# Optimization experiments

Hardware: AMD Instinct MI355X
Metric: run time of the kernel (lower is better)

The kernel has to match this reference:

```python
import jax, jax.numpy as jnp
import numpy as np

N = 50000          # num nodes
E = 800000         # num edges
MUL = 32           # channel multiplicity per irrep
NB = 8             # number of radial basis functions
R_MAX = 1.0
AVG = 16.0         # avg_num_neighbors
SQ3 = 3.0 ** 0.5


def setup_inputs() -> dict:
    key = jax.random.key(0)
    k = jax.random.split(key, 12)
    inp = {
        "node_feats": jax.random.normal(k[0], (N, 4 * MUL), dtype=jnp.float32),   # 32x0e + 32x1o (mul_ir layout)
        "edge_vec": jax.random.normal(k[1], (E, 3), dtype=jnp.float32),
        "edge_length": jax.random.uniform(k[2], (E,), dtype=jnp.float32),
        "senders": jax.random.randint(k[3], (E,), 0, N, dtype=jnp.int32),
        "receivers": jax.random.randint(k[4], (E,), 0, N, dtype=jnp.int32),
        "num_nodes": N,
        # linear_up: per-irrep channel mixing (scalars, vectors)
        "W_up0": jax.random.normal(k[5], (MUL, MUL), dtype=jnp.float32),
        "W_up1": jax.random.normal(k[6], (MUL, MUL), dtype=jnp.float32),
        # radial MLP: NB -> 64 -> 64 -> weight_numel (4 paths * MUL)
        "mlp_w0": jax.random.normal(k[7], (NB, 64), dtype=jnp.float32) / NB ** 0.5,
        "mlp_b0": jnp.zeros((64,), dtype=jnp.float32),
        "mlp_w1": jax.random.normal(k[8], (64, 64), dtype=jnp.float32) / 8.0,
        "mlp_b1": jnp.zeros((64,), dtype=jnp.float32),
        "mlp_w2": jax.random.normal(k[9], (64, 4 * MUL), dtype=jnp.float32) / 8.0,
        "mlp_b2": jnp.zeros((4 * MUL,), dtype=jnp.float32),
        # final linear: mid irreps 64x0e + 64x1o -> 32x0e + 32x1o
        "W_out0": jax.random.normal(k[10], (2 * MUL, MUL), dtype=jnp.float32),
        "W_out1": jax.random.normal(k[11], (2 * MUL, MUL), dtype=jnp.float32),
    }
    return inp


def _radial_embedding(r):
    # gaussian soft-one-hot, matches _radial_embedding(function_type='gaussian')
    x = jnp.clip(r / R_MAX, 0.0, 1.0)
    centers = jnp.arange(NB, dtype=jnp.float32) / (NB - 1)
    sigma = 1.0 / (NB - 1)
    emb = jnp.exp(-0.5 * ((x[:, None] - centers[None, :]) / sigma) ** 2)
    emb = emb * (NB ** 0.5) * (r <= R_MAX).astype(jnp.float32)[:, None]
    return emb  # [E, NB]


def reference(node_feats, edge_vec, edge_length, senders, receivers, num_nodes,
              W_up0, W_up1, mlp_w0, mlp_b0, mlp_w1, mlp_b1, mlp_w2, mlp_b2,
              W_out0, W_out1):
    f32 = jnp.float32
    # --- edge spherical harmonics (lmax=1, normalize=True, component norm) ---
    rhat = edge_vec / (jnp.linalg.norm(edge_vec, axis=-1, keepdims=True) + 1e-12)
    Y1 = SQ3 * rhat                                             # [E,3]
    # --- radial weights ---
    emb = _radial_embedding(edge_length)                        # [E,NB]
    h = jax.nn.silu(emb @ mlp_w0 + mlp_b0)
    h = jax.nn.silu(h @ mlp_w1 + mlp_b1)
    w = (h @ mlp_w2 + mlp_b2).reshape(-1, 4, MUL)               # [E,4,MUL] per-path per-channel
    # --- linear_up (per-irrep channel mixing, fan-in normalized) ---
    s = node_feats[:, :MUL]                                     # [N,MUL] scalars 0e
    v = node_feats[:, MUL:].reshape(-1, MUL, 3)                 # [N,MUL,3] vectors 1o
    xs = (s @ W_up0) / f32(MUL) ** 0.5                          # [N,MUL]
    xv = jnp.einsum('nmc,mk->nkc', v, W_up1) / f32(MUL) ** 0.5  # [N,MUL,3]
    # --- gather senders ---
    ss = xs[senders]                                            # [E,MUL]
    vv = xv[senders]                                            # [E,MUL,3]
    # --- channelwise tensor product paths (filter = {0e,1o}) ---
    m0 = w[:, 0] * ss                                           # 0e x 0e -> 0e   [E,MUL]
    m1 = w[:, 1][:, :, None] * ss[:, :, None] * Y1[:, None, :]  # 0e x 1o -> 1o   [E,MUL,3]
    m2 = w[:, 2][:, :, None] * vv                               # 1o x 0e -> 1o   [E,MUL,3]
    m3 = w[:, 3] * (jnp.einsum('emc,ec->em', vv, Y1) / SQ3)     # 1o x 1o -> 0e   [E,MUL]
    mid_s = jnp.concatenate([m0, m3], axis=1)                   # [E,2*MUL]
    mid_v = jnp.concatenate([m1, m2], axis=1)                   # [E,2*MUL,3]
    # --- scatter-sum to receivers ---
    msg_s = jax.ops.segment_sum(mid_s, receivers, num_segments=num_nodes)   # [N,2*MUL]
    msg_v = jax.ops.segment_sum(mid_v, receivers, num_segments=num_nodes)   # [N,2*MUL,3]
    # --- final per-irrep linear ---
    out_s = (msg_s @ W_out0) / f32(2 * MUL) ** 0.5              # [N,MUL]
    out_v = jnp.einsum('nmc,mk->nkc', msg_v, W_out1) / f32(2 * MUL) ** 0.5  # [N,MUL,3]
    out = jnp.concatenate([out_s, out_v.reshape(-1, 3 * MUL)], axis=1)      # [N,4*MUL]
    return out / max(AVG, 1e-8)
```

## Files before the change

### kernel.cpp

```cpp
#include <hip/hip_runtime.h>
#include <math.h>

#define SQ3F   1.7320508075688772f
#define SQRT8F 2.8284271247461903f
#define OSCALE (1.0f / 128.0f)

__device__ __forceinline__ float fast_silu(float x) {
    return x * __builtin_amdgcn_rcpf(1.0f + __expf(-x));
}

__global__ __launch_bounds__(256) void tr_kernel(const float* __restrict__ w2,
                                                 float* __restrict__ w2t) {
    const int t = blockIdx.x * 256 + threadIdx.x;
    if (t < 8192) {
        const int o = t >> 6, i = t & 63;
        w2t[t] = w2[i * 128 + o];
    }
}

__global__ __launch_bounds__(256) void up_kernel(const float* __restrict__ nf,
                                                 const float* __restrict__ Wu0,
                                                 const float* __restrict__ Wu1,
                                                 float* __restrict__ xall, int N) {
    __shared__ float sW0[1024], sW1[1024];
    for (int i = threadIdx.x; i < 1024; i += 256) { sW0[i] = Wu0[i]; sW1[i] = Wu1[i]; }
    __syncthreads();
    const int t = blockIdx.x * 256 + threadIdx.x;
    const int n = t >> 5, k = t & 31;
    if (n >= N) return;
    const float* row = nf + (size_t)n * 128;
    float a0 = 0.f, a1 = 0.f, a2 = 0.f, a3 = 0.f;
#pragma unroll
    for (int m = 0; m < 32; ++m) {
        const float wa = sW0[m * 32 + k], wb = sW1[m * 32 + k];
        a0 += row[m] * wa;
        a1 += row[32 + m * 3 + 0] * wb;
        a2 += row[32 + m * 3 + 1] * wb;
        a3 += row[32 + m * 3 + 2] * wb;
    }
    const float s = 0.17677669529663687f;
    float4 o; o.x = a0 * s; o.y = a1 * s; o.z = a2 * s; o.w = a3 * s;
    reinterpret_cast<float4*>(xall)[(size_t)n * 32 + k] = o;
}

__global__ __launch_bounds__(256) void hist_kernel(const int* __restrict__ rcv,
                                                   int* __restrict__ cnt, int E) {
    const int t = blockIdx.x * 256 + threadIdx.x;
    if (t < E) atomicAdd(&cnt[rcv[t]], 1);
}

__global__ __launch_bounds__(1024) void scan_kernel(const int* __restrict__ cnt,
                                                    int* __restrict__ off, int N, int E) {
    __shared__ int part[1024];
    const int t = threadIdx.x;
    const int CH = (N + 1023) / 1024;
    const int lo = t * CH;
    const int hi = (lo + CH < N) ? lo + CH : N;
    int s = 0;
    for (int i = lo; i < hi; ++i) s += cnt[i];
    part[t] = s;
    __syncthreads();
    for (int d = 1; d < 1024; d <<= 1) {
        const int v = (t >= d) ? part[t - d] : 0;
        __syncthreads();
        part[t] += v;
        __syncthreads();
    }
    int run = (t > 0) ? part[t - 1] : 0;
    for (int i = lo; i < hi; ++i) { off[i] = run; run += cnt[i]; }
    if (t == 0) off[N] = E;
}

__global__ __launch_bounds__(256) void scat_kernel(const int* __restrict__ rcv,
                                                   const int* __restrict__ off,
                                                   int* __restrict__ cur,
                                                   int* __restrict__ sid, int E) {
    const int t = blockIdx.x * 256 + threadIdx.x;
    if (t < E) {
        const int r = rcv[t];
        const int p = off[r] + atomicAdd(&cur[r], 1);
        sid[p] = t;
    }
}

__global__ __launch_bounds__(256) void wassign_kernel(const int* __restrict__ off,
                                                      int* __restrict__ wlo,
                                                      int* __restrict__ whi,
                                                      int N, int NW) {
    const int n = blockIdx.x * 256 + threadIdx.x;
    if (n < N) {
        int w = off[n] >> 6;
        if (w >= NW) w = NW - 1;
        atomicMin(&wlo[w], n);
        atomicMax(&whi[w], n);
    }
}

__global__ __launch_bounds__(64, 2) void ek4(const float* __restrict__ edge_vec,
                                             const float* __restrict__ edge_len,
                                             const int*  __restrict__ senders,
                                             const int*  __restrict__ receivers,
                                             const int*  __restrict__ sid,
                                             const int*  __restrict__ off,
                                             const int*  __restrict__ wlo,
                                             const int*  __restrict__ whi,
                                             const float* __restrict__ w0,
                                             const float* __restrict__ b0,
                                             const float* __restrict__ w1,
                                             const float* __restrict__ b1,
                                             const float* __restrict__ b2,
                                             const float* __restrict__ w2t,
                                             const float* __restrict__ Wo0,
                                             const float* __restrict__ Wo1,
                                             const float4* __restrict__ xall,
                                             float* __restrict__ outp,
                                             int E) {
    __shared__ float st[64][65];
    __shared__ int   rcvt[64];
    const int lane = threadIdx.x;
    const int w = blockIdx.x;
    const int nlo = wlo[w], nhi = whi[w];
    if (nhi < nlo) return;
    const int estart = off[nlo], eend = off[nhi + 1];
    if (estart >= eend) return;

    int   rprev = -1;
    float accA = 0.f, accB = 0.f;

    for (int bs = estart; bs < eend; bs += 64) {
        const int nv = (eend - bs < 64) ? (eend - bs) : 64;
        const int sp = (lane < nv) ? (bs + lane) : (eend - 1);
        const int e  = sid[sp];
        rcvt[lane] = receivers[e];

        const float ev0 = edge_vec[e * 3 + 0];
        const float ev1 = edge_vec[e * 3 + 1];
        const float ev2 = edge_vec[e * 3 + 2];
        const float r   = edge_len[e];
        const int  snd  = senders[e];

        const float nrm = sqrtf(ev0 * ev0 + ev1 * ev1 + ev2 * ev2) + 1e-12f;
        const float sc  = SQ3F * __builtin_amdgcn_rcpf(nrm);
        const float Y0 = ev0 * sc, Y1 = ev1 * sc, Y2 = ev2 * sc;

        const float xcl  = fminf(fmaxf(r, 0.0f), 1.0f);
        const float gate = (r <= 1.0f) ? SQRT8F : 0.0f;
        float emb[8];
#pragma unroll
        for (int i = 0; i < 8; ++i) {
            const float d = xcl * 7.0f - (float)i;
            emb[i] = __expf(-0.5f * d * d) * gate;
        }

        float h0[64];
#pragma unroll
        for (int o = 0; o < 64; ++o) {
            float a = b0[o];
#pragma unroll
            for (int i = 0; i < 8; ++i) a += emb[i] * w0[i * 64 + o];
            h0[o] = fast_silu(a);
        }

#pragma unroll 1
        for (int ob = 0; ob < 64; ob += 8) {
            float a[8];
#pragma unroll
            for (int u = 0; u < 8; ++u) a[u] = b1[ob + u];
#pragma unroll
            for (int i = 0; i < 64; ++i) {
                const float hv = h0[i];
#pragma unroll
                for (int u = 0; u < 8; ++u) a[u] += hv * w1[i * 64 + ob + u];
            }
#pragma unroll
            for (int u = 0; u < 8; ++u) st[ob + u][lane] = fast_silu(a[u]);
        }

        const float4* xrow = xall + (size_t)snd * 32;
        float outS[32], tA[32], oV[96];
#pragma unroll
        for (int k = 0; k < 32; ++k) { outS[k] = 0.f; tA[k] = 0.f; }
#pragma unroll
        for (int k = 0; k < 96; ++k) oV[k] = 0.f;

#pragma unroll 1
        for (int m = 0; m < 32; ++m) {
            const float* r0 = w2t + m * 64;
            const float* r1 = w2t + (32 + m) * 64;
            const float* r2 = w2t + (64 + m) * 64;
            const float* r3 = w2t + (96 + m) * 64;
            float d0 = b2[m], d1 = b2[32 + m], d2 = b2[64 + m], d3 = b2[96 + m];
#pragma unroll
            for (int i = 0; i < 64; ++i) {
                const float hv = st[i][lane];
                d0 += hv * r0[i]; d1 += hv * r1[i];
                d2 += hv * r2[i]; d3 += hv * r3[i];
            }
            const float4 g = xrow[m];
            const float ss = g.x;
            const float dv = g.y * Y0 + g.z * Y1 + g.w * Y2;
            const float a0 = d0 * ss;
            const float a3 = d3 * dv * (1.0f / SQ3F);
            const float t1 = d1 * ss;
            const float p0 = d2 * g.y, p1 = d2 * g.z, p2 = d2 * g.w;
            const float* wa = Wo0 + m * 32;
            const float* wb = Wo0 + (32 + m) * 32;
            const float* wc = Wo1 + m * 32;
            const float* wd = Wo1 + (32 + m) * 32;
#pragma unroll
            for (int k = 0; k < 32; ++k) {
                outS[k] += a0 * wa[k] + a3 * wb[k];
                tA[k]   += t1 * wc[k];
                const float wv = wd[k];
                oV[k * 3 + 0] += p0 * wv;
                oV[k * 3 + 1] += p1 * wv;
                oV[k * 3 + 2] += p2 * wv;
            }
        }
#pragma unroll
        for (int k = 0; k < 32; ++k) {
            oV[k * 3 + 0] += tA[k] * Y0;
            oV[k * 3 + 1] += tA[k] * Y1;
            oV[k * 3 + 2] += tA[k] * Y2;
        }

#pragma unroll
        for (int j = 0; j < 32; ++j) st[j][lane]      = outS[j];
#pragma unroll
        for (int j = 0; j < 32; ++j) st[32 + j][lane] = oV[j];
        __syncthreads();
        if (rprev < 0) rprev = rcvt[0];
        {
            int rA = rprev; float a = accA;
            for (int ee = 0; ee < nv; ++ee) {
                const int rc = rcvt[ee];
                if (rc != rA) {
                    outp[(size_t)rA * 128 + lane] = a * OSCALE;
                    a = 0.f; rA = rc;
                }
                a += st[lane][ee];
            }
            accA = a;
        }
        __syncthreads();

#pragma unroll
        for (int j = 0; j < 64; ++j) st[j][lane] = oV[32 + j];
        __syncthreads();
        {
            int rB = rprev; float b = accB;
            for (int ee = 0; ee < nv; ++ee) {
                const int rc = rcvt[ee];
                if (rc != rB) {
                    outp[(size_t)rB * 128 + 64 + lane] = b * OSCALE;
                    b = 0.f; rB = rc;
                }
                b += st[lane][ee];
            }
            accB = b; rprev = rB;
        }
        __syncthreads();
    }

    outp[(size_t)rprev * 128 + lane]      = accA * OSCALE;
    outp[(size_t)rprev * 128 + 64 + lane] = accB * OSCALE;
}

extern "C" void kernel_launch(void* const* d_in, const int* in_sizes, int n_in,
                              void* d_out, int out_size, void* d_ws, size_t ws_size,
                              hipStream_t stream) {
    const float* node_feats = (const float*)d_in[0];
    const float* edge_vec   = (const float*)d_in[1];
    const float* edge_len   = (const float*)d_in[2];
    const int*   senders    = (const int*)d_in[3];
    const int*   receivers  = (const int*)d_in[4];
    const float* W_up0  = (const float*)d_in[6];
    const float* W_up1  = (const float*)d_in[7];
    const float* mlp_w0 = (const float*)d_in[8];
    const float* mlp_b0 = (const float*)d_in[9];
    const float* mlp_w1 = (const float*)d_in[10];
    const float* mlp_b1 = (const float*)d_in[11];
    const float* mlp_w2 = (const float*)d_in[12];
    const float* mlp_b2 = (const float*)d_in[13];
    const float* W_out0 = (const float*)d_in[14];
    const float* W_out1 = (const float*)d_in[15];

    const int N  = in_sizes[0] / 128;
    const int E  = in_sizes[1] / 3;
    const int NW = (E + 63) / 64;

    float* xall = (float*)d_ws;
    float* w2t  = xall + (size_t)N * 128;
    int*   cnt  = (int*)(w2t + 8192);
    int*   off  = cnt + N;
    int*   cur  = off + N + 1;
    int*   sid  = cur + N;
    int*   wlo  = sid + E;
    int*   whi  = wlo + NW;

    tr_kernel<<<32, 256, 0, stream>>>(mlp_w2, w2t);
    up_kernel<<<(N * 32 + 255) / 256, 256, 0, stream>>>(node_feats, W_up0, W_up1, xall, N);

    hipMemsetAsync(cnt, 0, (size_t)(3 * N + 1) * sizeof(int), stream);
    hist_kernel<<<(E + 255) / 256, 256, 0, stream>>>(receivers, cnt, E);
    scan_kernel<<<1, 1024, 0, stream>>>(cnt, off, N, E);
    scat_kernel<<<(E + 255) / 256, 256, 0, stream>>>(receivers, off, cur, sid, E);

    hipMemsetAsync(wlo, 0x7f, (size_t)NW * sizeof(int), stream);
    hipMemsetAsync(whi, 0xff, (size_t)NW * sizeof(int), stream);
    wassign_kernel<<<(N + 255) / 256, 256, 0, stream>>>(off, wlo, whi, N, NW);

    hipMemsetAsync(d_out, 0, (size_t)out_size * sizeof(float), stream);
    ek4<<<NW, 64, 0, stream>>>(edge_vec, edge_len, senders, receivers, sid, off,
                               wlo, whi,
                               mlp_w0, mlp_b0, mlp_w1, mlp_b1, mlp_b2,
                               w2t, W_out0, W_out1,
                               (const float4*)xall, (float*)d_out, E);
}
```

Measured before the change: 2.495 ms.

## Keep hidden layer in registers and split output accumulation into two passes

The second MLP hidden layer h1 now stays in registers instead of going through shared memory, so the third MLP layer reads registers rather than LDS. The per-channel loop is split into two passes. The first pass builds the scalar outputs and the tA term, and the second pass recomputes the d2 path and builds the vector outputs. This avoids keeping outS, tA and all 96 oV accumulators live at the same time. It adds 64 live registers for h1, re-reads xrow, and adds an extra barrier, so register pressure at the launch bound of (64, 2) could cause spills.

New measurement: 3.274 ms. +31.2%, slower.

```diff
diff --git a/kernel.cpp b/kernel.cpp
--- a/kernel.cpp
+++ b/kernel.cpp
@@ -96,7 +96,7 @@
     }
 }
 
-__global__ __launch_bounds__(64, 2) void ek4(const float* __restrict__ edge_vec,
+__global__ __launch_bounds__(64, 2) void ek5(const float* __restrict__ edge_vec,
                                              const float* __restrict__ edge_len,
                                              const int*  __restrict__ senders,
                                              const int*  __restrict__ receivers,
@@ -161,7 +161,8 @@
             h0[o] = fast_silu(a);
         }
 
-#pragma unroll 1
+        float h1[64];
+#pragma unroll
         for (int ob = 0; ob < 64; ob += 8) {
             float a[8];
 #pragma unroll
@@ -173,28 +174,25 @@
                 for (int u = 0; u < 8; ++u) a[u] += hv * w1[i * 64 + ob + u];
             }
 #pragma unroll
-            for (int u = 0; u < 8; ++u) st[ob + u][lane] = fast_silu(a[u]);
+            for (int u = 0; u < 8; ++u) h1[ob + u] = fast_silu(a[u]);
         }
 
         const float4* xrow = xall + (size_t)snd * 32;
-        float outS[32], tA[32], oV[96];
+
+        float outS[32], tA[32];
 #pragma unroll
         for (int k = 0; k < 32; ++k) { outS[k] = 0.f; tA[k] = 0.f; }
-#pragma unroll
-        for (int k = 0; k < 96; ++k) oV[k] = 0.f;
 
 #pragma unroll 1
         for (int m = 0; m < 32; ++m) {
             const float* r0 = w2t + m * 64;
             const float* r1 = w2t + (32 + m) * 64;
-            const float* r2 = w2t + (64 + m) * 64;
             const float* r3 = w2t + (96 + m) * 64;
-            float d0 = b2[m], d1 = b2[32 + m], d2 = b2[64 + m], d3 = b2[96 + m];
+            float d0 = b2[m], d1 = b2[32 + m], d3 = b2[96 + m];
 #pragma unroll
             for (int i = 0; i < 64; ++i) {
-                const float hv = st[i][lane];
-                d0 += hv * r0[i]; d1 += hv * r1[i];
-                d2 += hv * r2[i]; d3 += hv * r3[i];
+                const float hv = h1[i];
+                d0 += hv * r0[i]; d1 += hv * r1[i]; d3 += hv * r3[i];
             }
             const float4 g = xrow[m];
             const float ss = g.x;
@@ -202,30 +200,47 @@
             const float a0 = d0 * ss;
             const float a3 = d3 * dv * (1.0f / SQ3F);
             const float t1 = d1 * ss;
-            const float p0 = d2 * g.y, p1 = d2 * g.z, p2 = d2 * g.w;
             const float* wa = Wo0 + m * 32;
             const float* wb = Wo0 + (32 + m) * 32;
             const float* wc = Wo1 + m * 32;
-            const float* wd = Wo1 + (32 + m) * 32;
 #pragma unroll
             for (int k = 0; k < 32; ++k) {
                 outS[k] += a0 * wa[k] + a3 * wb[k];
                 tA[k]   += t1 * wc[k];
+            }
+        }
+
+        __syncthreads();
+#pragma unroll
+        for (int j = 0; j < 32; ++j) st[j][lane] = outS[j];
+
+        float oV[96];
+#pragma unroll
+        for (int k = 0; k < 32; ++k) {
+            const float t = tA[k];
+            oV[k * 3 + 0] = t * Y0;
+            oV[k * 3 + 1] = t * Y1;
+            oV[k * 3 + 2] = t * Y2;
+        }
+
+#pragma unroll 1
+        for (int m = 0; m < 32; ++m) {
+            const float* r2 = w2t + (64 + m) * 64;
+            float d2 = b2[64 + m];
+#pragma unroll
+            for (int i = 0; i < 64; ++i) d2 += h1[i] * r2[i];
+            const float4 g = xrow[m];
+            const float p0 = d2 * g.y, p1 = d2 * g.z, p2 = d2 * g.w;
+            const float* wd = Wo1 + (32 + m) * 32;
+#pragma unroll
+            for (int k = 0; k < 32; ++k) {
                 const float wv = wd[k];
                 oV[k * 3 + 0] += p0 * wv;
                 oV[k * 3 + 1] += p1 * wv;
                 oV[k * 3 + 2] += p2 * wv;
             }
         }
-#pragma unroll
-        for (int k = 0; k < 32; ++k) {
-            oV[k * 3 + 0] += tA[k] * Y0;
-            oV[k * 3 + 1] += tA[k] * Y1;
-            oV[k * 3 + 2] += tA[k] * Y2;
-        }
-
-#pragma unroll
-        for (int j = 0; j < 32; ++j) st[j][lane]      = outS[j];
+
 #pragma unroll
         for (int j = 0; j < 32; ++j) st[32 + j][lane] = oV[j];
         __syncthreads();
@@ -311,7 +326,7 @@
     wassign_kernel<<<(N + 255) / 256, 256, 0, stream>>>(off, wlo, whi, N, NW);
 
     hipMemsetAsync(d_out, 0, (size_t)out_size * sizeof(float), stream);
-    ek4<<<NW, 64, 0, stream>>>(edge_vec, edge_len, senders, receivers, sid, off,
+    ek5<<<NW, 64, 0, stream>>>(edge_vec, edge_len, senders, receivers, sid, off,
                                wlo, whi,
                                mlp_w0, mlp_b0, mlp_w1, mlp_b1, mlp_b2,
                                w2t, W_out0, W_out1,
```
